# Optimization experiments

Hardware: AMD Instinct MI355X
Metric: run time of the kernel (lower is better)

Reference implementation:

```python
import jax, jax.numpy as jnp
import numpy as np

N = 100000
E = 1600000
D = 128


def setup_inputs() -> dict:
    key = jax.random.key(0)
    k1, k2, k3 = jax.random.split(key, 3)
    indices = jax.random.randint(k1, (2, E), 0, N, dtype=jnp.int64)
    values = jax.random.normal(k2, (E,), dtype=jnp.float32)
    b = jax.random.normal(k3, (N, D), dtype=jnp.float32)
    return {"indices": indices, "values": values, "n": N, "b": b}


def reference(indices, values, n, b):
    # Sparse COO SpMM: out[r] = sum_{e: row[e]==r} values[e] * b[col[e]]
    row, col = indices[0], indices[1]
    contrib = values[:, None] * b[col]          # [E, D] gather-multiply
    out = jax.ops.segment_sum(contrib, row, num_segments=n)  # [N, D] scatter-add
    return out
```

## Files before the change

kernel.cpp:

```cpp
#include <hip/hip_runtime.h>
#include <hip/hip_fp16.h>


#define D_DIM 128
#define RPB 64
#define RPB_SHIFT 6
#define MAXB 2048
#define CAP_LDS 1408
#define EPT 6
#define EPT1 8
#define OVF_MAX 65536

typedef float fx4 __attribute__((ext_vector_type(4)));

__global__ __launch_bounds__(256) void convert_b_kernel(
        const float* __restrict__ b, __half* __restrict__ bh, int n8) {
    int i = blockIdx.x * blockDim.x + threadIdx.x;
    if (i >= n8) return;
    const float4* b4 = (const float4*)b;
    float4 a0 = b4[2 * i];
    float4 a1 = b4[2 * i + 1];
    union { __half2 h[4]; uint4 u; } pk;
    pk.h[0] = __floats2half2_rn(a0.x, a0.y);
    pk.h[1] = __floats2half2_rn(a0.z, a0.w);
    pk.h[2] = __floats2half2_rn(a1.x, a1.y);
    pk.h[3] = __floats2half2_rn(a1.z, a1.w);
    ((uint4*)bh)[i] = pk.u;
}

__global__ __launch_bounds__(1024) void phase1_partition(
        const int* __restrict__ rows,
        const int* __restrict__ cols,
        const float* __restrict__ vals,
        int* __restrict__ bucket_cnt,
        int2* __restrict__ packed,
        int* __restrict__ ovf_cnt,
        int* __restrict__ ovf_list,
        int E, int nb, int cap, int chunk) {
    __shared__ int hist[MAXB];
    int tid = threadIdx.x;
    int start = blockIdx.x * chunk;
    int end = start + chunk; if (end > E) end = E;

    for (int i = tid; i < nb; i += 1024) hist[i] = 0;
    __syncthreads();

    int rr[EPT1]; int cc[EPT1]; float vv[EPT1];
    int ne = 0;
    for (int e = start + tid; e < end; e += 1024) {
        int r = rows[e];
        if (ne < EPT1) { rr[ne] = r; cc[ne] = cols[e]; vv[ne] = vals[e]; }
        ++ne;
        atomicAdd(&hist[r >> RPB_SHIFT], 1);
    }
    __syncthreads();

    for (int bkt = tid; bkt < nb; bkt += 1024) {
        int c = hist[bkt];
        hist[bkt] = (c > 0) ? atomicAdd(&bucket_cnt[bkt], c) : 0;
    }
    __syncthreads();

    int j = 0;
    for (int e = start + tid; e < end; e += 1024, ++j) {
        int r, c; float v;
        if (j < EPT1) { r = rr[j]; c = cc[j]; v = vv[j]; }
        else          { r = rows[e]; c = cols[e]; v = vals[e]; }
        int bkt = r >> RPB_SHIFT;
        int local = atomicAdd(&hist[bkt], 1);
        if (local < cap) {
            int key = ((r & (RPB - 1)) << 17) | c;
            packed[(size_t)bkt * cap + local] = make_int2(key, __float_as_int(v));
        } else {
            int k = atomicAdd(ovf_cnt, 1);
            if (k < OVF_MAX) ovf_list[k] = e;
        }
    }
}

template <bool HALF>
__global__ __launch_bounds__(256) void phase2_sort_gather(
        const int* __restrict__ bucket_cnt,
        const int2* __restrict__ packed,
        const __half* __restrict__ bh,
        const float* __restrict__ b,
        float* __restrict__ out,
        int cap, int N) {
    __shared__ int2 sorted[CAP_LDS];
    __shared__ int hist[RPB];
    __shared__ int offs[RPB + 1];
    __shared__ int cursor[RPB];

    int bucket = blockIdx.x;
    int tid = threadIdx.x;

    int cnt = bucket_cnt[bucket];
    if (cnt > cap) cnt = cap;
    const int2* pk = packed + (size_t)bucket * cap;

    if (tid < RPB) hist[tid] = 0;
    __syncthreads();

    int2 ev[EPT];
    int  rl[EPT];
    int ne = 0;
    for (int i = tid; i < cnt; i += 256) {
        int2 e = pk[i];
        ev[ne] = e;
        rl[ne] = ((unsigned)e.x) >> 17;
        atomicAdd(&hist[rl[ne]], 1);
        ++ne;
    }
    __syncthreads();

    for (int d = 1; d < RPB; d <<= 1) {
        int t = (tid < RPB && tid >= d) ? hist[tid - d] : 0;
        __syncthreads();
        if (tid < RPB) hist[tid] += t;
        __syncthreads();
    }
    if (tid == 0) offs[0] = 0;
    if (tid < RPB) {
        offs[tid + 1] = hist[tid];
        cursor[tid] = (tid == 0) ? 0 : hist[tid - 1];
    }
    __syncthreads();

    for (int j = 0; j < ne; ++j) {
        int pos = atomicAdd(&cursor[rl[j]], 1);
        sorted[pos] = make_int2(ev[j].x & 0x1FFFF, ev[j].y);
    }
    __syncthreads();

    int g = tid >> 5;
    int glane = tid & 31;
    int r0 = bucket << RPB_SHIFT;
    for (int k = 0; k < 8; ++k) {
        int rr = g * 8 + k;
        int start = offs[rr];
        int num = offs[rr + 1] - start;
        float4 acc = make_float4(0.f, 0.f, 0.f, 0.f);
        for (int base = 0; base < num; base += 8) {
#pragma unroll
            for (int j = 0; j < 8; ++j) {
                int idx = base + j;
                int sidx = start + ((idx < num) ? idx : (num - 1));
                int2 e = sorted[sidx];
                float v = (idx < num) ? __int_as_float(e.y) : 0.f;
                if (HALF) {
                    uint2 hv = ((const uint2*)(bh + (size_t)e.x * D_DIM))[glane];
                    __half2* hp = (__half2*)&hv;
                    float2 f0 = __half22float2(hp[0]);
                    float2 f1 = __half22float2(hp[1]);
                    acc.x += v * f0.x;
                    acc.y += v * f0.y;
                    acc.z += v * f1.x;
                    acc.w += v * f1.y;
                } else {
                    float4 bv = ((const float4*)(b + (size_t)e.x * D_DIM))[glane];
                    acc.x += v * bv.x;
                    acc.y += v * bv.y;
                    acc.z += v * bv.z;
                    acc.w += v * bv.w;
                }
            }
        }
        int r = r0 + rr;
        if (r < N) {
            fx4 av = {acc.x, acc.y, acc.z, acc.w};
            __builtin_nontemporal_store(av, (fx4*)(out + (size_t)r * D_DIM) + glane);
        }
    }
}

__global__ void fixup_kernel(const int* __restrict__ ovf_cnt,
                             const int* __restrict__ ovf_list,
                             const int* __restrict__ rows,
                             const int* __restrict__ cols,
                             const float* __restrict__ vals,
                             const float* __restrict__ b,
                             float* __restrict__ out) {
    int items = *ovf_cnt;
    if (items > OVF_MAX) items = OVF_MAX;
    int gsz  = (gridDim.x * blockDim.x) >> 5;
    int gid  = (blockIdx.x * blockDim.x + threadIdx.x) >> 5;
    int lane = threadIdx.x & 31;
    for (int i = gid; i < items; i += gsz) {
        int e = ovf_list[i];
        int r = rows[e];
        int c = cols[e];
        float v = vals[e];
        float4 bv = ((const float4*)(b + (size_t)c * D_DIM))[lane];
        float* op = out + (size_t)r * D_DIM + (size_t)lane * 4;
        atomicAdd(op + 0, v * bv.x);
        atomicAdd(op + 1, v * bv.y);
        atomicAdd(op + 2, v * bv.z);
        atomicAdd(op + 3, v * bv.w);
    }
}

__global__ void spmm_atomic_kernel(const int* __restrict__ rows,
                                   const int* __restrict__ cols,
                                   const float* __restrict__ vals,
                                   const float* __restrict__ b,
                                   float* __restrict__ out, int E) {
    int t = blockIdx.x * blockDim.x + threadIdx.x;
    int e = t >> 5;
    if (e >= E) return;
    int lane = t & 31;
    int r = rows[e];
    int c = cols[e];
    float v = vals[e];
    float4 bv = ((const float4*)(b + (size_t)c * D_DIM))[lane];
    float* op = out + (size_t)r * D_DIM + (size_t)lane * 4;
    atomicAdd(op + 0, v * bv.x);
    atomicAdd(op + 1, v * bv.y);
    atomicAdd(op + 2, v * bv.z);
    atomicAdd(op + 3, v * bv.w);
}

extern "C" void kernel_launch(void* const* d_in, const int* in_sizes, int n_in,
                              void* d_out, int out_size, void* d_ws, size_t ws_size,
                              hipStream_t stream) {
    const int*   indices = (const int*)d_in[0];
    const float* vals    = (const float*)d_in[1];
    const float* b       = (const float*)d_in[3];
    float*       out     = (float*)d_out;

    int E = in_sizes[1];
    int N = out_size / D_DIM;
    const int* rows = indices;
    const int* cols = indices + E;

    int nb = (N + RPB - 1) >> RPB_SHIFT;
    int avg = (nb > 0) ? E / nb : 0;
    int cap = CAP_LDS;

    size_t fixed      = (size_t)nb * 4 + 4 + (size_t)OVF_MAX * 4;
    size_t bh_off     = (fixed + 255) & ~(size_t)255;
    size_t bh_bytes   = (size_t)N * D_DIM * 2;
    size_t packed_h   = (bh_off + bh_bytes + 255) & ~(size_t)255;
    size_t packed_f   = bh_off;
    size_t need_h     = packed_h + (size_t)nb * cap * 8;
    size_t need_f     = packed_f + (size_t)nb * cap * 8;

    bool okBase = (nb <= MAXB) && (N <= 131072) && (cap > avg + avg / 8);
    bool useHalf = okBase && (ws_size >= need_h);
    bool useF32  = okBase && !useHalf && (ws_size >= need_f);

    if (!useHalf && !useF32) {
        (void)hipMemsetAsync(d_out, 0, (size_t)out_size * sizeof(float), stream);
        long long total = (long long)E * 32;
        int blocks = (int)((total + 255) / 256);
        spmm_atomic_kernel<<<blocks, 256, 0, stream>>>(rows, cols, vals, b, out, E);
        return;
    }

    char* w = (char*)d_ws;
    int*    bucket_cnt = (int*)w;
    int*    ovf_cnt    = (int*)(w + (size_t)nb * 4);
    int*    ovf_list   = (int*)(w + (size_t)nb * 4 + 4);
    __half* bh         = (__half*)(w + bh_off);
    int2*   packed     = (int2*)(w + (useHalf ? packed_h : packed_f));

    (void)hipMemsetAsync(bucket_cnt, 0, (size_t)nb * 4 + 4, stream);

    if (useHalf) {
        int n8 = N * D_DIM / 8;
        convert_b_kernel<<<(n8 + 255) / 256, 256, 0, stream>>>(b, bh, n8);
    }

    const int P1_WGS = 256;
    int chunk = (E + P1_WGS - 1) / P1_WGS;
    phase1_partition<<<P1_WGS, 1024, 0, stream>>>(
        rows, cols, vals, bucket_cnt, packed, ovf_cnt, ovf_list, E, nb, cap, chunk);

    if (useHalf)
        phase2_sort_gather<true><<<nb, 256, 0, stream>>>(
            bucket_cnt, packed, bh, b, out, cap, N);
    else
        phase2_sort_gather<false><<<nb, 256, 0, stream>>>(
            bucket_cnt, packed, bh, b, out, cap, N);

    fixup_kernel<<<8, 256, 0, stream>>>(ovf_cnt, ovf_list, rows, cols, vals, b, out);
}
```

Measured before the change: 215.3 us.

## Split partitioning into coarse 256-row bins then fine 64-row buckets

Partitioning now runs in two passes. Pass one scatters edges into 391 coarse bins of 256 rows, so the per-block histogram is small and global writes are less scattered. Pass two stages each bin in LDS and splits it into four 64-row buckets with contiguous writes. The coarse buffer shares workspace with the half-precision copy of b, so less workspace is needed, and overflow entries now carry row, col and value directly. The cost is an extra kernel launch plus a second read and write of every edge.

```diff
diff --git a/kernel.cpp b/kernel.cpp
--- a/kernel.cpp
+++ b/kernel.cpp
@@ -5,11 +5,15 @@
 #define D_DIM 128
 #define RPB 64
 #define RPB_SHIFT 6
+#define CRB 256
+#define CRB_SHIFT 8
+#define MAXCB 512
+#define CCAP 4608
 #define MAXB 2048
 #define CAP_LDS 1408
 #define EPT 6
 #define EPT1 8
-#define OVF_MAX 65536
+#define OVF_T 8192
 
 typedef float fx4 __attribute__((ext_vector_type(4)));
 
@@ -28,21 +32,21 @@
     ((uint4*)bh)[i] = pk.u;
 }
 
-__global__ __launch_bounds__(1024) void phase1_partition(
+__global__ __launch_bounds__(1024) void p1_coarse(
         const int* __restrict__ rows,
         const int* __restrict__ cols,
         const float* __restrict__ vals,
-        int* __restrict__ bucket_cnt,
-        int2* __restrict__ packed,
+        int* __restrict__ coarse_cnt,
+        int2* __restrict__ coarse,
         int* __restrict__ ovf_cnt,
-        int* __restrict__ ovf_list,
-        int E, int nb, int cap, int chunk) {
-    __shared__ int hist[MAXB];
+        int* __restrict__ ovf3,
+        int E, int ncb, int ccap, int chunk) {
+    __shared__ int hist[MAXCB];
     int tid = threadIdx.x;
     int start = blockIdx.x * chunk;
     int end = start + chunk; if (end > E) end = E;
 
-    for (int i = tid; i < nb; i += 1024) hist[i] = 0;
+    for (int i = tid; i < ncb; i += 1024) hist[i] = 0;
     __syncthreads();
 
     int rr[EPT1]; int cc[EPT1]; float vv[EPT1];
@@ -51,13 +55,13 @@
         int r = rows[e];
         if (ne < EPT1) { rr[ne] = r; cc[ne] = cols[e]; vv[ne] = vals[e]; }
         ++ne;
-        atomicAdd(&hist[r >> RPB_SHIFT], 1);
-    }
-    __syncthreads();
-
-    for (int bkt = tid; bkt < nb; bkt += 1024) {
-        int c = hist[bkt];
-        hist[bkt] = (c > 0) ? atomicAdd(&bucket_cnt[bkt], c) : 0;
+        atomicAdd(&hist[r >> CRB_SHIFT], 1);
+    }
+    __syncthreads();
+
+    for (int bin = tid; bin < ncb; bin += 1024) {
+        int c = hist[bin];
+        hist[bin] = (c > 0) ? atomicAdd(&coarse_cnt[bin], c) : 0;
     }
     __syncthreads();
 
@@ -66,14 +70,103 @@
         int r, c; float v;
         if (j < EPT1) { r = rr[j]; c = cc[j]; v = vv[j]; }
         else          { r = rows[e]; c = cols[e]; v = vals[e]; }
-        int bkt = r >> RPB_SHIFT;
-        int local = atomicAdd(&hist[bkt], 1);
-        if (local < cap) {
-            int key = ((r & (RPB - 1)) << 17) | c;
-            packed[(size_t)bkt * cap + local] = make_int2(key, __float_as_int(v));
+        int bin = r >> CRB_SHIFT;
+        int local = atomicAdd(&hist[bin], 1);
+        if (local < ccap) {
+            coarse[(size_t)bin * ccap + local] =
+                make_int2(((r & (CRB - 1)) << 17) | c, __float_as_int(v));
         } else {
             int k = atomicAdd(ovf_cnt, 1);
-            if (k < OVF_MAX) ovf_list[k] = e;
+            if (k < OVF_T) {
+                ovf3[3 * k] = r; ovf3[3 * k + 1] = c;
+                ovf3[3 * k + 2] = __float_as_int(v);
+            }
+        }
+    }
+}
+
+__global__ __launch_bounds__(1024) void p2_fine(
+        const int* __restrict__ coarse_cnt,
+        const int2* __restrict__ coarse,
+        int* __restrict__ bucket_cnt,
+        int2* __restrict__ packed,
+        int* __restrict__ ovf_cnt,
+        int* __restrict__ ovf3,
+        int ccap, int cap, int nb) {
+    __shared__ int2 stage[CCAP];
+    __shared__ int hist4[4];
+    __shared__ int loff[5];
+    __shared__ int cur[4];
+
+    int bin = blockIdx.x;
+    int tid = threadIdx.x;
+    int lane = tid & 63;
+    int cnt = coarse_cnt[bin];
+    if (cnt > ccap) cnt = ccap;
+    const int2* cb = coarse + (size_t)bin * ccap;
+
+    if (tid < 4) hist4[tid] = 0;
+
+    int h0 = 0, h1 = 0, h2 = 0, h3 = 0;
+    for (int i = tid; i < cnt; i += 1024) {
+        int f = (cb[i].x >> 23) & 3;
+        h0 += (f == 0); h1 += (f == 1); h2 += (f == 2); h3 += (f == 3);
+    }
+    for (int off = 32; off; off >>= 1) {
+        h0 += __shfl_down(h0, off); h1 += __shfl_down(h1, off);
+        h2 += __shfl_down(h2, off); h3 += __shfl_down(h3, off);
+    }
+    __syncthreads();
+    if (lane == 0) {
+        atomicAdd(&hist4[0], h0); atomicAdd(&hist4[1], h1);
+        atomicAdd(&hist4[2], h2); atomicAdd(&hist4[3], h3);
+    }
+    __syncthreads();
+    if (tid == 0) {
+        int o = 0;
+        for (int k = 0; k < 4; ++k) { loff[k] = o; cur[k] = o; o += hist4[k]; }
+        loff[4] = o;
+    }
+    __syncthreads();
+
+    for (int i = tid; i < cnt; i += 1024) {
+        int2 e = cb[i];
+        int f = (e.x >> 23) & 3;
+        int p = 0;
+        for (int k = 0; k < 4; ++k) {
+            unsigned long long m = __ballot(f == k);
+            if (f == k) {
+                int leader = __ffsll((unsigned long long)m) - 1;
+                int base = 0;
+                if (lane == leader) base = atomicAdd(&cur[k], (int)__popcll(m));
+                base = __shfl(base, leader);
+                p = base + (int)__popcll(m & ((1ULL << lane) - 1ULL));
+            }
+        }
+        stage[p] = e;
+    }
+    __syncthreads();
+
+    int fb0 = bin << (CRB_SHIFT - RPB_SHIFT);
+    for (int k = 0; k < 4; ++k) {
+        int bkt = fb0 + k;
+        if (bkt >= nb) break;
+        int s = loff[k];
+        int run = loff[k + 1] - s;
+        int w = (run > cap) ? cap : run;
+        for (int i = tid; i < w; i += 1024) {
+            int2 e = stage[s + i];
+            packed[(size_t)bkt * cap + i] = make_int2(e.x & 0x7FFFFF, e.y);
+        }
+        if (tid == 0) bucket_cnt[bkt] = w;
+        for (int i = cap + tid; i < run; i += 1024) {
+            int2 e = stage[s + i];
+            int k2 = atomicAdd(ovf_cnt, 1);
+            if (k2 < OVF_T) {
+                int r = (bin << CRB_SHIFT) | ((unsigned)e.x >> 17);
+                ovf3[3 * k2] = r; ovf3[3 * k2 + 1] = e.x & 0x1FFFF;
+                ovf3[3 * k2 + 2] = e.y;
+            }
         }
     }
 }
@@ -173,23 +266,72 @@
     }
 }
 
+__global__ __launch_bounds__(1024) void phase1_partition(
+        const int* __restrict__ rows,
+        const int* __restrict__ cols,
+        const float* __restrict__ vals,
+        int* __restrict__ bucket_cnt,
+        int2* __restrict__ packed,
+        int* __restrict__ ovf_cnt,
+        int* __restrict__ ovf3,
+        int E, int nb, int cap, int chunk) {
+    __shared__ int hist[MAXB];
+    int tid = threadIdx.x;
+    int start = blockIdx.x * chunk;
+    int end = start + chunk; if (end > E) end = E;
+
+    for (int i = tid; i < nb; i += 1024) hist[i] = 0;
+    __syncthreads();
+
+    int rr[EPT1]; int cc[EPT1]; float vv[EPT1];
+    int ne = 0;
+    for (int e = start + tid; e < end; e += 1024) {
+        int r = rows[e];
+        if (ne < EPT1) { rr[ne] = r; cc[ne] = cols[e]; vv[ne] = vals[e]; }
+        ++ne;
+        atomicAdd(&hist[r >> RPB_SHIFT], 1);
+    }
+    __syncthreads();
+
+    for (int bkt = tid; bkt < nb; bkt += 1024) {
+        int c = hist[bkt];
+        hist[bkt] = (c > 0) ? atomicAdd(&bucket_cnt[bkt], c) : 0;
+    }
+    __syncthreads();
+
+    int j = 0;
+    for (int e = start + tid; e < end; e += 1024, ++j) {
+        int r, c; float v;
+        if (j < EPT1) { r = rr[j]; c = cc[j]; v = vv[j]; }
+        else          { r = rows[e]; c = cols[e]; v = vals[e]; }
+        int bkt = r >> RPB_SHIFT;
+        int local = atomicAdd(&hist[bkt], 1);
+        if (local < cap) {
+            int key = ((r & (RPB - 1)) << 17) | c;
+            packed[(size_t)bkt * cap + local] = make_int2(key, __float_as_int(v));
+        } else {
+            int k = atomicAdd(ovf_cnt, 1);
+            if (k < OVF_T) {
+                ovf3[3 * k] = r; ovf3[3 * k + 1] = c;
+                ovf3[3 * k + 2] = __float_as_int(v);
+            }
+        }
+    }
+}
+
 __global__ void fixup_kernel(const int* __restrict__ ovf_cnt,
-                             const int* __restrict__ ovf_list,
-                             const int* __restrict__ rows,
-                             const int* __restrict__ cols,
-                             const float* __restrict__ vals,
+                             const int* __restrict__ ovf3,
                              const float* __restrict__ b,
                              float* __restrict__ out) {
     int items = *ovf_cnt;
-    if (items > OVF_MAX) items = OVF_MAX;
+    if (items > OVF_T) items = OVF_T;
     int gsz  = (gridDim.x * blockDim.x) >> 5;
     int gid  = (blockIdx.x * blockDim.x + threadIdx.x) >> 5;
     int lane = threadIdx.x & 31;
     for (int i = gid; i < items; i += gsz) {
-        int e = ovf_list[i];
-        int r = rows[e];
-        int c = cols[e];
-        float v = vals[e];
+        int r = ovf3[3 * i];
+        int c = ovf3[3 * i + 1];
+        float v = __int_as_float(ovf3[3 * i + 2]);
         float4 bv = ((const float4*)(b + (size_t)c * D_DIM))[lane];
         float* op = out + (size_t)r * D_DIM + (size_t)lane * 4;
         atomicAdd(op + 0, v * bv.x);
@@ -232,13 +374,57 @@
     const int* rows = indices;
     const int* cols = indices + E;
 
-    int nb = (N + RPB - 1) >> RPB_SHIFT;
-    int avg = (nb > 0) ? E / nb : 0;
+    int nb  = (N + RPB - 1) >> RPB_SHIFT;
+    int ncb = (N + CRB - 1) >> CRB_SHIFT;
+    int avg  = (nb  > 0) ? E / nb  : 0;
+    int cavg = (ncb > 0) ? E / ncb : 0;
     int cap = CAP_LDS;
-
-    size_t fixed      = (size_t)nb * 4 + 4 + (size_t)OVF_MAX * 4;
+    size_t bh_bytes = (size_t)N * D_DIM * 2;
+    int n8 = N * D_DIM / 8;
+
+    {
+        bool ok = (ncb <= MAXCB) && (N <= 131072) &&
+                  (cavg + cavg / 8 <= CCAP) && (cap > avg + avg / 8);
+        size_t fixedN = (size_t)ncb * 4 + (size_t)nb * 4 + 4 + (size_t)OVF_T * 12;
+        size_t pk_off = (fixedN + 255) & ~(size_t)255;
+        size_t un_off = (pk_off + (size_t)nb * cap * 8 + 255) & ~(size_t)255;
+        size_t coarse_bytes = (size_t)ncb * CCAP * 8;
+        size_t un_bytes = coarse_bytes > bh_bytes ? coarse_bytes : bh_bytes;
+        if (ok && ws_size >= un_off + un_bytes) {
+            char* w = (char*)d_ws;
+            int*    coarse_cnt = (int*)w;
+            int*    bucket_cnt = (int*)(w + (size_t)ncb * 4);
+            int*    ovf_cnt    = (int*)(w + (size_t)ncb * 4 + (size_t)nb * 4);
+            int*    ovf3       = (int*)(w + (size_t)ncb * 4 + (size_t)nb * 4 + 4);
+            int2*   packed     = (int2*)(w + pk_off);
+            int2*   coarse     = (int2*)(w + un_off);
+            __half* bh         = (__half*)(w + un_off);
+
+            (void)hipMemsetAsync(coarse_cnt, 0,
+                                 (size_t)ncb * 4 + (size_t)nb * 4 + 4, stream);
+
+            const int P1_WGS = 256;
+            int chunk = (E + P1_WGS - 1) / P1_WGS;
+            p1_coarse<<<P1_WGS, 1024, 0, stream>>>(
+                rows, cols, vals, coarse_cnt, coarse, ovf_cnt, ovf3,
+                E, ncb, CCAP, chunk);
+
+            p2_fine<<<ncb, 1024, 0, stream>>>(
+                coarse_cnt, coarse, bucket_cnt, packed, ovf_cnt, ovf3,
+                CCAP, cap, nb);
+
+            convert_b_kernel<<<(n8 + 255) / 256, 256, 0, stream>>>(b, bh, n8);
+
+            phase2_sort_gather<true><<<nb, 256, 0, stream>>>(
+                bucket_cnt, packed, bh, b, out, cap, N);
+
+            fixup_kernel<<<8, 256, 0, stream>>>(ovf_cnt, ovf3, b, out);
+            return;
+        }
+    }
+
+    size_t fixed      = (size_t)nb * 4 + 4 + (size_t)OVF_T * 12;
     size_t bh_off     = (fixed + 255) & ~(size_t)255;
-    size_t bh_bytes   = (size_t)N * D_DIM * 2;
     size_t packed_h   = (bh_off + bh_bytes + 255) & ~(size_t)255;
     size_t packed_f   = bh_off;
     size_t need_h     = packed_h + (size_t)nb * cap * 8;
@@ -259,21 +445,19 @@
     char* w = (char*)d_ws;
     int*    bucket_cnt = (int*)w;
     int*    ovf_cnt    = (int*)(w + (size_t)nb * 4);
-    int*    ovf_list   = (int*)(w + (size_t)nb * 4 + 4);
+    int*    ovf3       = (int*)(w + (size_t)nb * 4 + 4);
     __half* bh         = (__half*)(w + bh_off);
     int2*   packed     = (int2*)(w + (useHalf ? packed_h : packed_f));
 
     (void)hipMemsetAsync(bucket_cnt, 0, (size_t)nb * 4 + 4, stream);
 
-    if (useHalf) {
-        int n8 = N * D_DIM / 8;
+    if (useHalf)
         convert_b_kernel<<<(n8 + 255) / 256, 256, 0, stream>>>(b, bh, n8);
-    }
 
     const int P1_WGS = 256;
     int chunk = (E + P1_WGS - 1) / P1_WGS;
     phase1_partition<<<P1_WGS, 1024, 0, stream>>>(
-        rows, cols, vals, bucket_cnt, packed, ovf_cnt, ovf_list, E, nb, cap, chunk);
+        rows, cols, vals, bucket_cnt, packed, ovf_cnt, ovf3, E, nb, cap, chunk);
 
     if (useHalf)
         phase2_sort_gather<true><<<nb, 256, 0, stream>>>(
@@ -282,5 +466,5 @@
         phase2_sort_gather<false><<<nb, 256, 0, stream>>>(
             bucket_cnt, packed, bh, b, out, cap, N);
 
-    fixup_kernel<<<8, 256, 0, stream>>>(ovf_cnt, ovf_list, rows, cols, vals, b, out);
-}
+    fixup_kernel<<<8, 256, 0, stream>>>(ovf_cnt, ovf3, b, out);
+}
```

Result: slower. 228.2 us (+6.0%).
